# Optimization experiments

Measured on AMD Instinct MI355X. Metric: run time of the kernel, lower is better.

Reference implementation:

```python
import jax, jax.numpy as jnp
import numpy as np

# Model constants (from init_kwargs)
N_EMBD = 1024
N_HEAD = 16
HEAD_DIM = N_EMBD // N_HEAD  # 64
SEQ = 32       # new tokens (ds.input_ids)
PAST = 32768   # cached tokens (ds.past)
NEG = -10000.0 # module uses -1e4, not -inf


def setup_inputs() -> dict:
    key = jax.random.key(0)
    ks = jax.random.split(key, 5)
    return {
        "x": jax.random.normal(ks[0], (SEQ, N_EMBD), jnp.float32),
        "layer_past": jax.random.normal(ks[1], (2, N_HEAD, PAST, HEAD_DIM), jnp.float32) * 0.02,
        "w_attn": jax.random.normal(ks[2], (N_EMBD, 3 * N_EMBD), jnp.float32) * 0.02,
        "b_attn": jnp.zeros((3 * N_EMBD,), jnp.float32),
        "w_proj": jax.random.normal(ks[3], (N_EMBD, N_EMBD), jnp.float32) * 0.02,
        "b_proj": jnp.zeros((N_EMBD,), jnp.float32),
        "seq_len": SEQ,
        "past_len": PAST,
    }


def reference(x, layer_past, w_attn, b_attn, w_proj, b_proj, seq_len, past_len):
    # c_attn (Conv1D): x @ W + b, W is [nx, nf]
    qkv = x @ w_attn + b_attn                      # [S, 3E]
    qkv = qkv.reshape(seq_len, 3, N_EMBD)
    # split_heads: [S, E] -> [S, H, D] -> [H, S, D]
    def split(t):
        return t.reshape(seq_len, N_HEAD, HEAD_DIM).transpose(1, 0, 2)
    q, k, v = split(qkv[:, 0]), split(qkv[:, 1]), split(qkv[:, 2])
    # KV-cache concat along time
    key_full = jnp.concatenate([layer_past[0], k], axis=1)   # [H, P+S, D]
    val_full = jnp.concatenate([layer_past[1], v], axis=1)   # [H, P+S, D]
    present = jnp.stack([key_full, val_full])                # [2, H, P+S, D]
    tot_len = past_len + seq_len
    # scores
    w = jnp.einsum("hsd,htd->hst", q, key_full) / float(np.sqrt(HEAD_DIM))
    # causal mask: query at abs position past+i sees keys 0..past+i
    mask = jnp.arange(tot_len)[None, :] <= (past_len + jnp.arange(seq_len))[:, None]
    w = jnp.where(mask[None, :, :], w, NEG)
    w = jax.nn.softmax(w, axis=-1)
    a = jnp.einsum("hst,htd->hsd", w, val_full)              # [H, S, D]
    # merge_heads: [H, S, D] -> [S, H, D] -> [S, E]
    a = a.transpose(1, 0, 2).reshape(seq_len, N_EMBD)
    out = a @ w_proj + b_proj                                # [S, E]
    return (out, present)
```

## Files before the change

kernel.cpp:

```cpp
#include <hip/hip_runtime.h>

#define HEADS 16
#define SEQL 32
#define HD 64
#define PASTN 32768
#define TOTN 32800
#define NE 1024
#define CHUNK 512
#define NPC 64
#define NCHUNK 65
#define KT 32
#define SLDP 36
#define NEGV -10000.0f

__global__ __launch_bounds__(256) void qkv_kernel(
    const float* __restrict__ x, const float* __restrict__ w,
    const float* __restrict__ b, float* __restrict__ qws,
    float* __restrict__ present)
{
    int idx = blockIdx.x * 256 + threadIdx.x;
    int s = idx / 3072;
    int col = idx - s * 3072;
    const float* xr = x + s * NE;
    float a0 = 0.f, a1 = 0.f, a2 = 0.f, a3 = 0.f;
    for (int k = 0; k < NE; k += 4) {
        a0 = fmaf(xr[k + 0], w[(k + 0) * 3072 + col], a0);
        a1 = fmaf(xr[k + 1], w[(k + 1) * 3072 + col], a1);
        a2 = fmaf(xr[k + 2], w[(k + 2) * 3072 + col], a2);
        a3 = fmaf(xr[k + 3], w[(k + 3) * 3072 + col], a3);
    }
    float acc = b[col] + ((a0 + a1) + (a2 + a3));
    int g = col >> 10;
    int e = col & 1023;
    int h = e >> 6, d = e & 63;
    if (g == 0)
        qws[(h * SEQL + s) * HD + d] = acc;
    else
        present[(((g - 1) * HEADS + h) * TOTN + PASTN + s) * HD + d] = acc;
}

__global__ __launch_bounds__(256) void attn_partial(
    const float* __restrict__ past, const float* __restrict__ qws,
    float* __restrict__ present, float* __restrict__ opart,
    float* __restrict__ mws, float* __restrict__ lws)
{
    int h = blockIdx.x / NCHUNK;
    int c = blockIdx.x - h * NCHUNK;
    __shared__ __align__(16) float Qs[SEQL][HD];
    __shared__ __align__(16) float Ks[KT][HD];
    __shared__ __align__(16) float Vs[KT][HD];
    __shared__ __align__(16) float Ss[SEQL][SLDP];
    __shared__ float mrow[SEQL], lrow[SEQL], arow[SEQL];
    int tid = threadIdx.x;

    for (int i = tid; i < SEQL * 16; i += 256) {
        int q = i >> 4, s4 = i & 15;
        *(float4*)&Qs[q][s4 * 4] = *(const float4*)&qws[(h * SEQL + q) * HD + s4 * 4];
    }
    if (tid < SEQL) { mrow[tid] = -3e38f; lrow[tid] = 0.f; }

    float acc[8];
#pragma unroll
    for (int j = 0; j < 8; ++j) acc[j] = 0.f;

    int lk = tid & 31;
    int q0 = (tid >> 5) * 4;
    int nkeys = (c < NPC) ? CHUNK : SEQL;
    int kstart = c * CHUNK;
    __syncthreads();

    for (int t0 = 0; t0 < nkeys; t0 += KT) {
        if (c < NPC) {
#pragma unroll
            for (int rep = 0; rep < 2; ++rep) {
                int i = tid + rep * 256;
                int row = i >> 4, s4 = i & 15;
                int grow = kstart + t0 + row;
                float4 kk = *(const float4*)&past[(h * PASTN + grow) * HD + s4 * 4];
                float4 vv = *(const float4*)&past[((HEADS + h) * PASTN + grow) * HD + s4 * 4];
                *(float4*)&present[(h * TOTN + grow) * HD + s4 * 4] = kk;
                *(float4*)&present[((HEADS + h) * TOTN + grow) * HD + s4 * 4] = vv;
                int sl = (s4 ^ (row & 7)) * 4;
                *(float4*)&Ks[row][sl] = kk;
                *(float4*)&Vs[row][sl] = vv;
            }
        } else {
#pragma unroll
            for (int rep = 0; rep < 2; ++rep) {
                int i = tid + rep * 256;
                int row = i >> 4, s4 = i & 15;
                int grow = PASTN + t0 + row;
                float4 kk = *(const float4*)&present[(h * TOTN + grow) * HD + s4 * 4];
                float4 vv = *(const float4*)&present[((HEADS + h) * TOTN + grow) * HD + s4 * 4];
                int sl = (s4 ^ (row & 7)) * 4;
                *(float4*)&Ks[row][sl] = kk;
                *(float4*)&Vs[row][sl] = vv;
            }
        }
        __syncthreads();

        {
            float s0 = 0.f, s1 = 0.f, s2 = 0.f, s3 = 0.f;
            int xr = lk & 7;
#pragma unroll
            for (int d4 = 0; d4 < 16; ++d4) {
                float4 kk = *(const float4*)&Ks[lk][(d4 ^ xr) * 4];
                float4 r0 = *(const float4*)&Qs[q0 + 0][d4 * 4];
                float4 r1 = *(const float4*)&Qs[q0 + 1][d4 * 4];
                float4 r2 = *(const float4*)&Qs[q0 + 2][d4 * 4];
                float4 r3 = *(const float4*)&Qs[q0 + 3][d4 * 4];
                s0 = fmaf(r0.x, kk.x, s0); s0 = fmaf(r0.y, kk.y, s0);
                s0 = fmaf(r0.z, kk.z, s0); s0 = fmaf(r0.w, kk.w, s0);
                s1 = fmaf(r1.x, kk.x, s1); s1 = fmaf(r1.y, kk.y, s1);
                s1 = fmaf(r1.z, kk.z, s1); s1 = fmaf(r1.w, kk.w, s1);
                s2 = fmaf(r2.x, kk.x, s2); s2 = fmaf(r2.y, kk.y, s2);
                s2 = fmaf(r2.z, kk.z, s2); s2 = fmaf(r2.w, kk.w, s2);
                s3 = fmaf(r3.x, kk.x, s3); s3 = fmaf(r3.y, kk.y, s3);
                s3 = fmaf(r3.z, kk.z, s3); s3 = fmaf(r3.w, kk.w, s3);
            }
            s0 *= 0.125f; s1 *= 0.125f; s2 *= 0.125f; s3 *= 0.125f;
            if (c == NPC) {
                if (lk > q0 + 0) s0 = NEGV;
                if (lk > q0 + 1) s1 = NEGV;
                if (lk > q0 + 2) s2 = NEGV;
                if (lk > q0 + 3) s3 = NEGV;
            }
            Ss[q0 + 0][lk] = s0;
            Ss[q0 + 1][lk] = s1;
            Ss[q0 + 2][lk] = s2;
            Ss[q0 + 3][lk] = s3;
        }
        __syncthreads();

        {
            int q = tid >> 3, sub = tid & 7;
            float4 sv = *(const float4*)&Ss[q][sub * 4];
            float mt = fmaxf(fmaxf(sv.x, sv.y), fmaxf(sv.z, sv.w));
            mt = fmaxf(mt, __shfl_xor(mt, 1));
            mt = fmaxf(mt, __shfl_xor(mt, 2));
            mt = fmaxf(mt, __shfl_xor(mt, 4));
            float mold = mrow[q];
            float mnew = fmaxf(mold, mt);
            float4 p;
            p.x = __expf(sv.x - mnew);
            p.y = __expf(sv.y - mnew);
            p.z = __expf(sv.z - mnew);
            p.w = __expf(sv.w - mnew);
            *(float4*)&Ss[q][sub * 4] = p;
            float ls = (p.x + p.y) + (p.z + p.w);
            ls += __shfl_xor(ls, 1);
            ls += __shfl_xor(ls, 2);
            ls += __shfl_xor(ls, 4);
            if (sub == 0) {
                float alpha = __expf(mold - mnew);
                lrow[q] = lrow[q] * alpha + ls;
                mrow[q] = mnew;
                arow[q] = alpha;
            }
        }
        __syncthreads();

        {
            int dq = lk >> 2, dr = lk & 3;
#pragma unroll
            for (int j = 0; j < 4; ++j) {
                float aj = arow[q0 + j];
                acc[2 * j] *= aj;
                acc[2 * j + 1] *= aj;
            }
#pragma unroll
            for (int t4 = 0; t4 < KT; t4 += 4) {
                float va[4], vb[4];
#pragma unroll
                for (int u = 0; u < 4; ++u) {
                    int t = t4 + u;
                    int sl = ((dq ^ (t & 7)) * 4) + dr;
                    va[u] = Vs[t][sl];
                    vb[u] = Vs[t][sl + 32];
                }
#pragma unroll
                for (int j = 0; j < 4; ++j) {
                    float4 pv = *(const float4*)&Ss[q0 + j][t4];
                    float u1 = acc[2 * j], u2 = acc[2 * j + 1];
                    u1 = fmaf(pv.x, va[0], u1); u1 = fmaf(pv.y, va[1], u1);
                    u1 = fmaf(pv.z, va[2], u1); u1 = fmaf(pv.w, va[3], u1);
                    u2 = fmaf(pv.x, vb[0], u2); u2 = fmaf(pv.y, vb[1], u2);
                    u2 = fmaf(pv.z, vb[2], u2); u2 = fmaf(pv.w, vb[3], u2);
                    acc[2 * j] = u1; acc[2 * j + 1] = u2;
                }
            }
        }
        __syncthreads();
    }

    if (tid < SEQL) {
        mws[(h * NCHUNK + c) * SEQL + tid] = mrow[tid];
        lws[(h * NCHUNK + c) * SEQL + tid] = lrow[tid];
    }
#pragma unroll
    for (int j = 0; j < 4; ++j) {
        int q = q0 + j;
        opart[((h * NCHUNK + c) * SEQL + q) * HD + lk] = acc[2 * j];
        opart[((h * NCHUNK + c) * SEQL + q) * HD + lk + 32] = acc[2 * j + 1];
    }
}

__global__ __launch_bounds__(64) void attn_reduce(
    const float* __restrict__ opart, const float* __restrict__ mws,
    const float* __restrict__ lws, float* __restrict__ aws)
{
    int h = blockIdx.x >> 5;
    int q = blockIdx.x & 31;
    int d = threadIdx.x;
    float M = -3e38f;
    for (int c = 0; c < NCHUNK; ++c)
        M = fmaxf(M, mws[(h * NCHUNK + c) * SEQL + q]);
    float L = 0.f, o = 0.f;
    for (int c = 0; c < NCHUNK; ++c) {
        float wgt = __expf(mws[(h * NCHUNK + c) * SEQL + q] - M);
        L = fmaf(lws[(h * NCHUNK + c) * SEQL + q], wgt, L);
        o = fmaf(opart[((h * NCHUNK + c) * SEQL + q) * HD + d], wgt, o);
    }
    aws[q * NE + h * HD + d] = o / L;
}

__global__ __launch_bounds__(256) void proj_kernel(
    const float* __restrict__ aws, const float* __restrict__ w,
    const float* __restrict__ b, float* __restrict__ out)
{
    int idx = blockIdx.x * 256 + threadIdx.x;
    int s = idx >> 10, e = idx & 1023;
    const float* ar = aws + s * NE;
    float a0 = 0.f, a1 = 0.f, a2 = 0.f, a3 = 0.f;
    for (int k = 0; k < NE; k += 4) {
        a0 = fmaf(ar[k + 0], w[(k + 0) * NE + e], a0);
        a1 = fmaf(ar[k + 1], w[(k + 1) * NE + e], a1);
        a2 = fmaf(ar[k + 2], w[(k + 2) * NE + e], a2);
        a3 = fmaf(ar[k + 3], w[(k + 3) * NE + e], a3);
    }
    out[idx] = b[e] + ((a0 + a1) + (a2 + a3));
}

extern "C" void kernel_launch(void* const* d_in, const int* in_sizes, int n_in,
                              void* d_out, int out_size, void* d_ws, size_t ws_size,
                              hipStream_t stream) {
    const float* x      = (const float*)d_in[0];
    const float* past   = (const float*)d_in[1];
    const float* w_attn = (const float*)d_in[2];
    const float* b_attn = (const float*)d_in[3];
    const float* w_proj = (const float*)d_in[4];
    const float* b_proj = (const float*)d_in[5];

    float* out     = (float*)d_out;
    float* present = out + SEQL * NE;

    float* wsf   = (float*)d_ws;
    float* qws   = wsf;
    float* aws   = wsf + 32768;
    float* mws   = wsf + 65536;
    float* lws   = mws + 33280;
    float* opart = lws + 33280;

    qkv_kernel<<<(SEQL * 3072) / 256, 256, 0, stream>>>(x, w_attn, b_attn, qws, present);
    attn_partial<<<HEADS * NCHUNK, 256, 0, stream>>>(past, qws, present, opart, mws, lws);
    attn_reduce<<<HEADS * SEQL, 64, 0, stream>>>(opart, mws, lws, aws);
    proj_kernel<<<(SEQL * NE) / 256, 256, 0, stream>>>(aws, w_proj, b_proj, out);
}
```

Before: 622.5 us.

## Enlarge attention chunks and key tiles, use 4x4 register tiling in score/PV loops

Doubles the chunk size to 1024 keys and the key tile to 64, halving the number of partial blocks (33 per head) and the reduce work. The QK and PV inner loops switch to 4x4 register tiles with float4 shared-memory loads on padded rows instead of XOR swizzling, but only half the threads (128) do compute. The QKV and projection GEMV loops now load x as float4 with unroll hints. The main risks are fewer blocks (528) to hide the memory-bound KV copy, and idle threads during compute.

```diff
diff --git a/kernel.cpp b/kernel.cpp
--- a/kernel.cpp
+++ b/kernel.cpp
@@ -6,11 +6,11 @@
 #define PASTN 32768
 #define TOTN 32800
 #define NE 1024
-#define CHUNK 512
-#define NPC 64
-#define NCHUNK 65
-#define KT 32
-#define SLDP 36
+#define CHUNK 1024
+#define NPC 32
+#define NCHUNK 33
+#define KT 64
+#define LDP 68
 #define NEGV -10000.0f
 
 __global__ __launch_bounds__(256) void qkv_kernel(
@@ -21,13 +21,16 @@
     int idx = blockIdx.x * 256 + threadIdx.x;
     int s = idx / 3072;
     int col = idx - s * 3072;
-    const float* xr = x + s * NE;
+    const float4* x4 = (const float4*)(x + s * NE);
     float a0 = 0.f, a1 = 0.f, a2 = 0.f, a3 = 0.f;
-    for (int k = 0; k < NE; k += 4) {
-        a0 = fmaf(xr[k + 0], w[(k + 0) * 3072 + col], a0);
-        a1 = fmaf(xr[k + 1], w[(k + 1) * 3072 + col], a1);
-        a2 = fmaf(xr[k + 2], w[(k + 2) * 3072 + col], a2);
-        a3 = fmaf(xr[k + 3], w[(k + 3) * 3072 + col], a3);
+#pragma unroll 8
+    for (int k4 = 0; k4 < NE / 4; ++k4) {
+        float4 xv = x4[k4];
+        const float* wp = w + (k4 * 4) * 3072 + col;
+        a0 = fmaf(xv.x, wp[0],        a0);
+        a1 = fmaf(xv.y, wp[3072],     a1);
+        a2 = fmaf(xv.z, wp[2 * 3072], a2);
+        a3 = fmaf(xv.w, wp[3 * 3072], a3);
     }
     float acc = b[col] + ((a0 + a1) + (a2 + a3));
     int g = col >> 10;
@@ -46,10 +49,10 @@
 {
     int h = blockIdx.x / NCHUNK;
     int c = blockIdx.x - h * NCHUNK;
-    __shared__ __align__(16) float Qs[SEQL][HD];
-    __shared__ __align__(16) float Ks[KT][HD];
-    __shared__ __align__(16) float Vs[KT][HD];
-    __shared__ __align__(16) float Ss[SEQL][SLDP];
+    __shared__ __align__(16) float Qs[SEQL][LDP];
+    __shared__ __align__(16) float Ks[KT][LDP];
+    __shared__ __align__(16) float Vs[KT][LDP];
+    __shared__ __align__(16) float Ss[SEQL][LDP];
     __shared__ float mrow[SEQL], lrow[SEQL], arow[SEQL];
     int tid = threadIdx.x;
 
@@ -59,20 +62,20 @@
     }
     if (tid < SEQL) { mrow[tid] = -3e38f; lrow[tid] = 0.f; }
 
-    float acc[8];
-#pragma unroll
-    for (int j = 0; j < 8; ++j) acc[j] = 0.f;
-
-    int lk = tid & 31;
-    int q0 = (tid >> 5) * 4;
-    int nkeys = (c < NPC) ? CHUNK : SEQL;
+    float4 acc4[4];
+#pragma unroll
+    for (int j = 0; j < 4; ++j) acc4[j] = make_float4(0.f, 0.f, 0.f, 0.f);
+
+    int qg = tid >> 4;
+    int lg = tid & 15;
+    int nkeys = (c < NPC) ? CHUNK : KT;
     int kstart = c * CHUNK;
     __syncthreads();
 
     for (int t0 = 0; t0 < nkeys; t0 += KT) {
         if (c < NPC) {
 #pragma unroll
-            for (int rep = 0; rep < 2; ++rep) {
+            for (int rep = 0; rep < 4; ++rep) {
                 int i = tid + rep * 256;
                 int row = i >> 4, s4 = i & 15;
                 int grow = kstart + t0 + row;
@@ -80,74 +83,82 @@
                 float4 vv = *(const float4*)&past[((HEADS + h) * PASTN + grow) * HD + s4 * 4];
                 *(float4*)&present[(h * TOTN + grow) * HD + s4 * 4] = kk;
                 *(float4*)&present[((HEADS + h) * TOTN + grow) * HD + s4 * 4] = vv;
-                int sl = (s4 ^ (row & 7)) * 4;
-                *(float4*)&Ks[row][sl] = kk;
-                *(float4*)&Vs[row][sl] = vv;
+                *(float4*)&Ks[row][s4 * 4] = kk;
+                *(float4*)&Vs[row][s4 * 4] = vv;
             }
         } else {
+            float* vz = &Vs[SEQL][0];
+            for (int i = tid; i < (KT - SEQL) * LDP; i += 256) vz[i] = 0.f;
 #pragma unroll
             for (int rep = 0; rep < 2; ++rep) {
                 int i = tid + rep * 256;
                 int row = i >> 4, s4 = i & 15;
-                int grow = PASTN + t0 + row;
+                int grow = PASTN + row;
                 float4 kk = *(const float4*)&present[(h * TOTN + grow) * HD + s4 * 4];
                 float4 vv = *(const float4*)&present[((HEADS + h) * TOTN + grow) * HD + s4 * 4];
-                int sl = (s4 ^ (row & 7)) * 4;
-                *(float4*)&Ks[row][sl] = kk;
-                *(float4*)&Vs[row][sl] = vv;
-            }
-        }
-        __syncthreads();
-
-        {
-            float s0 = 0.f, s1 = 0.f, s2 = 0.f, s3 = 0.f;
-            int xr = lk & 7;
+                *(float4*)&Ks[row][s4 * 4] = kk;
+                *(float4*)&Vs[row][s4 * 4] = vv;
+            }
+        }
+        __syncthreads();
+
+        if (tid < 128) {
+            float s[4][4];
+#pragma unroll
+            for (int j = 0; j < 4; ++j)
+#pragma unroll
+                for (int u = 0; u < 4; ++u) s[j][u] = 0.f;
 #pragma unroll
             for (int d4 = 0; d4 < 16; ++d4) {
-                float4 kk = *(const float4*)&Ks[lk][(d4 ^ xr) * 4];
-                float4 r0 = *(const float4*)&Qs[q0 + 0][d4 * 4];
-                float4 r1 = *(const float4*)&Qs[q0 + 1][d4 * 4];
-                float4 r2 = *(const float4*)&Qs[q0 + 2][d4 * 4];
-                float4 r3 = *(const float4*)&Qs[q0 + 3][d4 * 4];
-                s0 = fmaf(r0.x, kk.x, s0); s0 = fmaf(r0.y, kk.y, s0);
-                s0 = fmaf(r0.z, kk.z, s0); s0 = fmaf(r0.w, kk.w, s0);
-                s1 = fmaf(r1.x, kk.x, s1); s1 = fmaf(r1.y, kk.y, s1);
-                s1 = fmaf(r1.z, kk.z, s1); s1 = fmaf(r1.w, kk.w, s1);
-                s2 = fmaf(r2.x, kk.x, s2); s2 = fmaf(r2.y, kk.y, s2);
-                s2 = fmaf(r2.z, kk.z, s2); s2 = fmaf(r2.w, kk.w, s2);
-                s3 = fmaf(r3.x, kk.x, s3); s3 = fmaf(r3.y, kk.y, s3);
-                s3 = fmaf(r3.z, kk.z, s3); s3 = fmaf(r3.w, kk.w, s3);
-            }
-            s0 *= 0.125f; s1 *= 0.125f; s2 *= 0.125f; s3 *= 0.125f;
-            if (c == NPC) {
-                if (lk > q0 + 0) s0 = NEGV;
-                if (lk > q0 + 1) s1 = NEGV;
-                if (lk > q0 + 2) s2 = NEGV;
-                if (lk > q0 + 3) s3 = NEGV;
-            }
-            Ss[q0 + 0][lk] = s0;
-            Ss[q0 + 1][lk] = s1;
-            Ss[q0 + 2][lk] = s2;
-            Ss[q0 + 3][lk] = s3;
+                float4 qv[4], kv[4];
+#pragma unroll
+                for (int j = 0; j < 4; ++j)
+                    qv[j] = *(const float4*)&Qs[qg * 4 + j][d4 * 4];
+#pragma unroll
+                for (int u = 0; u < 4; ++u)
+                    kv[u] = *(const float4*)&Ks[lg + u * 16][d4 * 4];
+#pragma unroll
+                for (int j = 0; j < 4; ++j)
+#pragma unroll
+                    for (int u = 0; u < 4; ++u) {
+                        s[j][u] = fmaf(qv[j].x, kv[u].x, s[j][u]);
+                        s[j][u] = fmaf(qv[j].y, kv[u].y, s[j][u]);
+                        s[j][u] = fmaf(qv[j].z, kv[u].z, s[j][u]);
+                        s[j][u] = fmaf(qv[j].w, kv[u].w, s[j][u]);
+                    }
+            }
+#pragma unroll
+            for (int j = 0; j < 4; ++j) {
+                int q = qg * 4 + j;
+#pragma unroll
+                for (int u = 0; u < 4; ++u) {
+                    float sv = s[j][u] * 0.125f;
+                    if (c == NPC && (lg + u * 16) > q) sv = NEGV;
+                    Ss[q][lg + u * 16] = sv;
+                }
+            }
         }
         __syncthreads();
 
         {
             int q = tid >> 3, sub = tid & 7;
-            float4 sv = *(const float4*)&Ss[q][sub * 4];
-            float mt = fmaxf(fmaxf(sv.x, sv.y), fmaxf(sv.z, sv.w));
+            float v[8];
+#pragma unroll
+            for (int i = 0; i < 8; ++i) v[i] = Ss[q][sub + 8 * i];
+            float mt = fmaxf(fmaxf(fmaxf(v[0], v[1]), fmaxf(v[2], v[3])),
+                             fmaxf(fmaxf(v[4], v[5]), fmaxf(v[6], v[7])));
             mt = fmaxf(mt, __shfl_xor(mt, 1));
             mt = fmaxf(mt, __shfl_xor(mt, 2));
             mt = fmaxf(mt, __shfl_xor(mt, 4));
             float mold = mrow[q];
             float mnew = fmaxf(mold, mt);
-            float4 p;
-            p.x = __expf(sv.x - mnew);
-            p.y = __expf(sv.y - mnew);
-            p.z = __expf(sv.z - mnew);
-            p.w = __expf(sv.w - mnew);
-            *(float4*)&Ss[q][sub * 4] = p;
-            float ls = (p.x + p.y) + (p.z + p.w);
+            float ls = 0.f;
+#pragma unroll
+            for (int i = 0; i < 8; ++i) {
+                float p = __expf(v[i] - mnew);
+                Ss[q][sub + 8 * i] = p;
+                ls += p;
+            }
             ls += __shfl_xor(ls, 1);
             ls += __shfl_xor(ls, 2);
             ls += __shfl_xor(ls, 4);
@@ -160,33 +171,37 @@
         }
         __syncthreads();
 
-        {
-            int dq = lk >> 2, dr = lk & 3;
+        if (tid < 128) {
 #pragma unroll
             for (int j = 0; j < 4; ++j) {
-                float aj = arow[q0 + j];
-                acc[2 * j] *= aj;
-                acc[2 * j + 1] *= aj;
-            }
-#pragma unroll
-            for (int t4 = 0; t4 < KT; t4 += 4) {
-                float va[4], vb[4];
-#pragma unroll
-                for (int u = 0; u < 4; ++u) {
-                    int t = t4 + u;
-                    int sl = ((dq ^ (t & 7)) * 4) + dr;
-                    va[u] = Vs[t][sl];
-                    vb[u] = Vs[t][sl + 32];
-                }
+                float aj = arow[qg * 4 + j];
+                acc4[j].x *= aj; acc4[j].y *= aj; acc4[j].z *= aj; acc4[j].w *= aj;
+            }
+#pragma unroll
+            for (int t4 = 0; t4 < 16; ++t4) {
+                float4 vv[4];
+#pragma unroll
+                for (int u = 0; u < 4; ++u)
+                    vv[u] = *(const float4*)&Vs[t4 * 4 + u][lg * 4];
 #pragma unroll
                 for (int j = 0; j < 4; ++j) {
-                    float4 pv = *(const float4*)&Ss[q0 + j][t4];
-                    float u1 = acc[2 * j], u2 = acc[2 * j + 1];
-                    u1 = fmaf(pv.x, va[0], u1); u1 = fmaf(pv.y, va[1], u1);
-                    u1 = fmaf(pv.z, va[2], u1); u1 = fmaf(pv.w, va[3], u1);
-                    u2 = fmaf(pv.x, vb[0], u2); u2 = fmaf(pv.y, vb[1], u2);
-                    u2 = fmaf(pv.z, vb[2], u2); u2 = fmaf(pv.w, vb[3], u2);
-                    acc[2 * j] = u1; acc[2 * j + 1] = u2;
+                    float4 p = *(const float4*)&Ss[qg * 4 + j][t4 * 4];
+                    acc4[j].x = fmaf(p.x, vv[0].x, acc4[j].x);
+                    acc4[j].x = fmaf(p.y, vv[1].x, acc4[j].x);
+                    acc4[j].x = fmaf(p.z, vv[2].x, acc4[j].x);
+                    acc4[j].x = fmaf(p.w, vv[3].x, acc4[j].x);
+                    acc4[j].y = fmaf(p.x, vv[0].y, acc4[j].y);
+                    acc4[j].y = fmaf(p.y, vv[1].y, acc4[j].y);
+                    acc4[j].y = fmaf(p.z, vv[2].y, acc4[j].y);
+                    acc4[j].y = fmaf(p.w, vv[3].y, acc4[j].y);
+                    acc4[j].z = fmaf(p.x, vv[0].z, acc4[j].z);
+                    acc4[j].z = fmaf(p.y, vv[1].z, acc4[j].z);
+                    acc4[j].z = fmaf(p.z, vv[2].z, acc4[j].z);
+                    acc4[j].z = fmaf(p.w, vv[3].z, acc4[j].z);
+                    acc4[j].w = fmaf(p.x, vv[0].w, acc4[j].w);
+                    acc4[j].w = fmaf(p.y, vv[1].w, acc4[j].w);
+                    acc4[j].w = fmaf(p.z, vv[2].w, acc4[j].w);
+                    acc4[j].w = fmaf(p.w, vv[3].w, acc4[j].w);
                 }
             }
         }
@@ -197,11 +212,12 @@
         mws[(h * NCHUNK + c) * SEQL + tid] = mrow[tid];
         lws[(h * NCHUNK + c) * SEQL + tid] = lrow[tid];
     }
-#pragma unroll
-    for (int j = 0; j < 4; ++j) {
-        int q = q0 + j;
-        opart[((h * NCHUNK + c) * SEQL + q) * HD + lk] = acc[2 * j];
-        opart[((h * NCHUNK + c) * SEQL + q) * HD + lk + 32] = acc[2 * j + 1];
+    if (tid < 128) {
+#pragma unroll
+        for (int j = 0; j < 4; ++j) {
+            int q = qg * 4 + j;
+            *(float4*)&opart[((h * NCHUNK + c) * SEQL + q) * HD + lg * 4] = acc4[j];
+        }
     }
 }
 
@@ -230,13 +246,16 @@
 {
     int idx = blockIdx.x * 256 + threadIdx.x;
     int s = idx >> 10, e = idx & 1023;
-    const float* ar = aws + s * NE;
+    const float4* a4 = (const float4*)(aws + s * NE);
     float a0 = 0.f, a1 = 0.f, a2 = 0.f, a3 = 0.f;
-    for (int k = 0; k < NE; k += 4) {
-        a0 = fmaf(ar[k + 0], w[(k + 0) * NE + e], a0);
-        a1 = fmaf(ar[k + 1], w[(k + 1) * NE + e], a1);
-        a2 = fmaf(ar[k + 2], w[(k + 2) * NE + e], a2);
-        a3 = fmaf(ar[k + 3], w[(k + 3) * NE + e], a3);
+#pragma unroll 8
+    for (int k4 = 0; k4 < NE / 4; ++k4) {
+        float4 xv = a4[k4];
+        const float* wp = w + (k4 * 4) * NE + e;
+        a0 = fmaf(xv.x, wp[0],      a0);
+        a1 = fmaf(xv.y, wp[NE],     a1);
+        a2 = fmaf(xv.z, wp[2 * NE], a2);
+        a3 = fmaf(xv.w, wp[3 * NE], a3);
     }
     out[idx] = b[e] + ((a0 + a1) + (a2 + a3));
 }
@@ -258,8 +277,8 @@
     float* qws   = wsf;
     float* aws   = wsf + 32768;
     float* mws   = wsf + 65536;
-    float* lws   = mws + 33280;
-    float* opart = lws + 33280;
+    float* lws   = mws + 16896;
+    float* opart = lws + 16896;
 
     qkv_kernel<<<(SEQL * 3072) / 256, 256, 0, stream>>>(x, w_attn, b_attn, qws, present);
     attn_partial<<<HEADS * NCHUNK, 256, 0, stream>>>(past, qws, present, opart, mws, lws);
```

Measured after the change: 579.7 us. 6.9% less time.
